# Kernel optimization log

Hardware: AMD Instinct MI355X
Metric: run time of the kernel (lower is better)

Reference implementation:

```python
import jax, jax.numpy as jnp
import numpy as np

B = 4096
IN_F = 4096
OUT_F = 4096
IN_Q = IN_F // 4
OUT_Q = OUT_F // 4


def setup_inputs() -> dict:
    key = jax.random.key(0)
    ks = jax.random.split(key, 9)
    scale = 1.0 / np.sqrt(IN_Q)
    inp = {"x": jax.random.normal(ks[0], (B, IN_F), dtype=jnp.float32)}
    for i, name in enumerate(["rr", "ri", "rj", "rk"]):
        inp[f"W_{name}"] = jax.random.uniform(ks[1 + i], (OUT_Q, IN_Q), dtype=jnp.float32, minval=-scale, maxval=scale)
        inp[f"b_{name}"] = jax.random.uniform(ks[5 + i], (OUT_Q,), dtype=jnp.float32, minval=-scale, maxval=scale)
    return inp


def reference(x, W_rr, W_ri, W_rj, W_rk, b_rr, b_ri, b_rj, b_rk):
    b = x.shape[0]
    # split into quaternion components: chunks c in {r,i,j,k}
    xs = x.reshape(b, 4, IN_Q)                       # [B, 4, IN_Q]
    W = jnp.stack([W_rr, W_ri, W_rj, W_rk])          # [4(lin), OUT_Q, IN_Q]
    bias = jnp.stack([b_rr, b_ri, b_rj, b_rk])       # [4(lin), OUT_Q]
    # all 16 linear applications in one batched GEMM: Y[b,c,q,:] = lin_q(x_c)
    Y = jnp.einsum('bci,qoi->bcqo', xs, W) + bias    # [B, 4, 4, OUT_Q]
    out_r = Y[:, 0, 0] - Y[:, 1, 1] - Y[:, 2, 2] - Y[:, 3, 3]
    out_i = Y[:, 0, 1] + Y[:, 1, 0] + Y[:, 2, 3] - Y[:, 3, 2]
    out_j = Y[:, 0, 2] - Y[:, 1, 3] + Y[:, 2, 0] + Y[:, 3, 1]
    out_k = Y[:, 0, 3] + Y[:, 1, 2] - Y[:, 2, 1] + Y[:, 3, 0]
    out = jnp.stack([out_r, out_i, out_j, out_k], axis=1)  # [B, 4, OUT_Q]
    return out.reshape(b, -1)                        # [B, OUT_F]
```

## Files before the change

kernel.cpp:

```cpp
#include <hip/hip_runtime.h>
#include <cstdint>
#include <cstddef>

#define MDIM 4096
#define NDIM 4096
#define KDIM 4096

typedef _Float16 half8  __attribute__((ext_vector_type(8)));
typedef float    floatx4 __attribute__((ext_vector_type(4)));

__device__ __constant__ int   d_qtab[16] = {0,1,2,3,  1,0,3,2,  2,3,0,1,  3,2,1,0};
__device__ __constant__ float d_stab[16] = {1.f,-1.f,-1.f,-1.f,
                                            1.f, 1.f, 1.f,-1.f,
                                            1.f,-1.f, 1.f, 1.f,
                                            1.f, 1.f,-1.f, 1.f};


__global__ void cast_x_kernel(const float* __restrict__ x, _Float16* __restrict__ xh) {
    int idx = blockIdx.x * 256 + threadIdx.x;
    const float4* src = (const float4*)x + (size_t)idx * 2;
    float4 a = src[0], b = src[1];
    half8 h = {(_Float16)a.x, (_Float16)a.y, (_Float16)a.z, (_Float16)a.w,
               (_Float16)b.x, (_Float16)b.y, (_Float16)b.z, (_Float16)b.w};
    ((half8*)xh)[idx] = h;
}

__global__ void cast_w_kernel(const float* __restrict__ W0, const float* __restrict__ W1,
                              const float* __restrict__ W2, const float* __restrict__ W3,
                              _Float16* __restrict__ Wh) {
    int idx = blockIdx.x * 256 + threadIdx.x;
    int e = idx << 3;
    int m = e >> 20;
    const float* Ws[4] = {W0, W1, W2, W3};
    const float* src = Ws[m] + (e & ((1 << 20) - 1));
    float4 a = *(const float4*)src;
    float4 b = *(const float4*)(src + 4);
    half8 h = {(_Float16)a.x, (_Float16)a.y, (_Float16)a.z, (_Float16)a.w,
               (_Float16)b.x, (_Float16)b.y, (_Float16)b.z, (_Float16)b.w};
    *(half8*)(Wh + e) = h;
}


__device__ __forceinline__ void gload_lds16(const _Float16* g, _Float16* l) {
    __builtin_amdgcn_global_load_lds(
        (const __attribute__((address_space(1))) unsigned int*)g,
        (__attribute__((address_space(3))) unsigned int*)l,
        16, 0, 0);
}

__global__ __launch_bounds__(256, 4) void gemm_kernel(
        const _Float16* __restrict__ A,
        const _Float16* __restrict__ Wh,
        const float* __restrict__ b0, const float* __restrict__ b1,
        const float* __restrict__ b2, const float* __restrict__ b3,
        float* __restrict__ C) {
    __shared__ _Float16 As[128 * 32];
    __shared__ _Float16 Bs[128 * 32];

    const int tid  = threadIdx.x;
    const int lane = tid & 63;
    const int wave = tid >> 6;
    const int wm = (wave & 1) * 64;
    const int wn = (wave >> 1) * 64;

    const int g = blockIdx.x;
    const int group_id = g >> 8;
    const int bm = group_id * 8 + (g & 7);
    const int bn = (g & 255) >> 3;
    const int m0 = bm * 128;
    const int n0 = bn * 128;
    const int comp = n0 >> 10;

    const int srow = tid >> 2;
    const int skc  = (((tid & 3) ^ ((srow >> 1) & 3))) * 8;
    const _Float16* Ag0 = A + (size_t)(m0 + srow) * KDIM + skc;
    const int brow = (n0 & 1023) + srow;

    _Float16* Asl0 = As + tid * 8;
    _Float16* Asl1 = As + 2048 + tid * 8;
    _Float16* Bsl0 = Bs + tid * 8;
    _Float16* Bsl1 = Bs + 2048 + tid * 8;

    floatx4 acc[4][4];
#pragma unroll
    for (int i = 0; i < 4; i++)
#pragma unroll
        for (int j = 0; j < 4; j++)
            acc[i][j] = (floatx4){0.f, 0.f, 0.f, 0.f};

    const int fr = lane & 15;
    const int q  = lane >> 4;
    const int slot8 = (q ^ ((fr >> 1) & 3)) * 8;

    for (int c = 0; c < 4; c++) {
        const int t = comp * 4 + c;
        const _Float16* Bg0 = Wh + ((size_t)d_qtab[t] << 20) + (size_t)brow * 1024 + skc;
        const _Float16* Ag  = Ag0 + c * 1024;
        const _Float16 s = (_Float16)d_stab[t];
        half8 sv = {s, s, s, s, s, s, s, s};

        for (int kk = 0; kk < 1024; kk += 32) {
            gload_lds16(Ag + kk, Asl0);
            gload_lds16(Ag + (size_t)64 * KDIM + kk, Asl1);
            gload_lds16(Bg0 + kk, Bsl0);
            gload_lds16(Bg0 + (size_t)64 * 1024 + kk, Bsl1);
            __syncthreads();

            half8 af[4], bf[4];
#pragma unroll
            for (int i = 0; i < 4; i++) {
                af[i] = *(const half8*)(As + (wm + i * 16 + fr) * 32 + slot8) * sv;
                bf[i] = *(const half8*)(Bs + (wn + i * 16 + fr) * 32 + slot8);
            }
#pragma unroll
            for (int i = 0; i < 4; i++)
#pragma unroll
                for (int j = 0; j < 4; j++)
                    acc[i][j] = __builtin_amdgcn_mfma_f32_16x16x32_f16(af[i], bf[j], acc[i][j], 0, 0, 0);

            __syncthreads();
        }
    }

    const int col   = lane & 15;
    const int rquad = (lane >> 4) * 4;
    const float* bs[4] = {b0, b1, b2, b3};
#pragma unroll
    for (int j = 0; j < 4; j++) {
        const int gn = n0 + wn + j * 16 + col;
        const int o  = gn & 1023;
        float bv = 0.f;
#pragma unroll
        for (int c = 0; c < 4; c++)
            bv += d_stab[comp * 4 + c] * bs[d_qtab[comp * 4 + c]][o];
#pragma unroll
        for (int i = 0; i < 4; i++) {
            const int gmb = m0 + wm + i * 16 + rquad;
#pragma unroll
            for (int r = 0; r < 4; r++)
                C[(size_t)(gmb + r) * NDIM + gn] = acc[i][j][r] + bv;
        }
    }
}

__global__ void fallback_kernel(const float* __restrict__ x,
                                const float* __restrict__ W0, const float* __restrict__ W1,
                                const float* __restrict__ W2, const float* __restrict__ W3,
                                const float* __restrict__ b0, const float* __restrict__ b1,
                                const float* __restrict__ b2, const float* __restrict__ b3,
                                float* __restrict__ out) {
    int idx = blockIdx.x * 256 + threadIdx.x;
    int m = idx >> 12, n = idx & 4095;
    int comp = n >> 10, o = n & 1023;
    const float* Ws[4] = {W0, W1, W2, W3};
    const float* bs[4] = {b0, b1, b2, b3};
    float acc = 0.f;
    for (int c = 0; c < 4; c++) {
        int t = comp * 4 + c;
        const float* wr = Ws[d_qtab[t]] + (size_t)o * 1024;
        const float* xr = x + (size_t)m * 4096 + c * 1024;
        float s = d_stab[t];
        float dot = 0.f;
        for (int i = 0; i < 1024; i += 4) {
            float4 wv = *(const float4*)(wr + i);
            float4 xv = *(const float4*)(xr + i);
            dot += wv.x * xv.x + wv.y * xv.y + wv.z * xv.z + wv.w * xv.w;
        }
        acc += s * dot + s * bs[d_qtab[t]][o];
    }
    out[idx] = acc;
}

extern "C" void kernel_launch(void* const* d_in, const int* in_sizes, int n_in,
                              void* d_out, int out_size, void* d_ws, size_t ws_size,
                              hipStream_t stream) {
    const float* x = (const float*)d_in[0];
    const float* W[4];
    const float* b[4];
    int wi = 0, bi = 0;
    for (int i = 1; i < n_in && i < 9; i++) {
        if (in_sizes[i] > 4096) { if (wi < 4) W[wi++] = (const float*)d_in[i]; }
        else                    { if (bi < 4) b[bi++] = (const float*)d_in[i]; }
    }
    float* out = (float*)d_out;

    const size_t xh_elems = (size_t)MDIM * KDIM;
    const size_t wh_elems = (size_t)4 * 1024 * 1024;
    const size_t needed = (xh_elems + wh_elems) * 2;

    if (ws_size < needed) {
        fallback_kernel<<<(MDIM * NDIM) / 256, 256, 0, stream>>>(
            x, W[0], W[1], W[2], W[3], b[0], b[1], b[2], b[3], out);
        return;
    }

    _Float16* xh = (_Float16*)d_ws;
    _Float16* Wh = xh + xh_elems;

    cast_x_kernel<<<(MDIM * KDIM) / (256 * 8), 256, 0, stream>>>(x, xh);
    cast_w_kernel<<<(4 * 1024 * 1024) / (256 * 8), 256, 0, stream>>>(W[0], W[1], W[2], W[3], Wh);
    gemm_kernel<<<(MDIM / 128) * (NDIM / 128), 256, 0, stream>>>(
        xh, Wh, b[0], b[1], b[2], b[3], out);
}
```

Measured before the change: 298.9 us.

## Switch to 32x32x16 MFMA, pre-negate weights, and merge cast kernels

The GEMM inner loop moves from 16x16x32 MFMA tiles to 32x32x16 tiles, using 2x2 accumulators of 16 floats per wave with new LDS fragment addressing and a new epilogue mapping. The per-fragment sign multiply is dropped by storing a negated copy of the fp16 weights and picking the positive or negative copy per quaternion term. The two cast kernels are merged into one launch that also writes the negated weights. This cuts per-iteration VALU work, LDS reads and one launch, in exchange for doubling the fp16 weight workspace and the extra writes in the prepass.

```diff
diff --git a/kernel.cpp b/kernel.cpp
--- a/kernel.cpp
+++ b/kernel.cpp
@@ -6,38 +6,43 @@
 #define NDIM 4096
 #define KDIM 4096
 
-typedef _Float16 half8  __attribute__((ext_vector_type(8)));
-typedef float    floatx4 __attribute__((ext_vector_type(4)));
+typedef _Float16 half8   __attribute__((ext_vector_type(8)));
+typedef float    floatx16 __attribute__((ext_vector_type(16)));
 
 __device__ __constant__ int   d_qtab[16] = {0,1,2,3,  1,0,3,2,  2,3,0,1,  3,2,1,0};
+__device__ __constant__ int   d_negtab[16] = {0,1,1,1,  0,0,0,1,  0,1,0,0,  0,0,1,0};
 __device__ __constant__ float d_stab[16] = {1.f,-1.f,-1.f,-1.f,
                                             1.f, 1.f, 1.f,-1.f,
                                             1.f,-1.f, 1.f, 1.f,
                                             1.f, 1.f,-1.f, 1.f};
 
-
-__global__ void cast_x_kernel(const float* __restrict__ x, _Float16* __restrict__ xh) {
-    int idx = blockIdx.x * 256 + threadIdx.x;
-    const float4* src = (const float4*)x + (size_t)idx * 2;
-    float4 a = src[0], b = src[1];
-    half8 h = {(_Float16)a.x, (_Float16)a.y, (_Float16)a.z, (_Float16)a.w,
-               (_Float16)b.x, (_Float16)b.y, (_Float16)b.z, (_Float16)b.w};
-    ((half8*)xh)[idx] = h;
-}
-
-__global__ void cast_w_kernel(const float* __restrict__ W0, const float* __restrict__ W1,
-                              const float* __restrict__ W2, const float* __restrict__ W3,
-                              _Float16* __restrict__ Wh) {
-    int idx = blockIdx.x * 256 + threadIdx.x;
-    int e = idx << 3;
-    int m = e >> 20;
-    const float* Ws[4] = {W0, W1, W2, W3};
-    const float* src = Ws[m] + (e & ((1 << 20) - 1));
-    float4 a = *(const float4*)src;
-    float4 b = *(const float4*)(src + 4);
-    half8 h = {(_Float16)a.x, (_Float16)a.y, (_Float16)a.z, (_Float16)a.w,
-               (_Float16)b.x, (_Float16)b.y, (_Float16)b.z, (_Float16)b.w};
-    *(half8*)(Wh + e) = h;
+__global__ void prepass_kernel(const float* __restrict__ x,
+                               const float* __restrict__ W0, const float* __restrict__ W1,
+                               const float* __restrict__ W2, const float* __restrict__ W3,
+                               _Float16* __restrict__ xh, _Float16* __restrict__ Wh) {
+    int b = blockIdx.x;
+    if (b < 8192) {
+        int idx = b * 256 + threadIdx.x;
+        const float4* src = (const float4*)x + (size_t)idx * 2;
+        float4 a = src[0], v = src[1];
+        half8 h = {(_Float16)a.x, (_Float16)a.y, (_Float16)a.z, (_Float16)a.w,
+                   (_Float16)v.x, (_Float16)v.y, (_Float16)v.z, (_Float16)v.w};
+        ((half8*)xh)[idx] = h;
+    } else {
+        int idx = (b - 8192) * 256 + threadIdx.x;
+        int e = idx << 3;
+        int m = e >> 20;
+        int off = e & ((1 << 20) - 1);
+        const float* Ws[4] = {W0, W1, W2, W3};
+        const float* src = Ws[m] + off;
+        float4 a = *(const float4*)src;
+        float4 v = *(const float4*)(src + 4);
+        half8 hp = {(_Float16)a.x, (_Float16)a.y, (_Float16)a.z, (_Float16)a.w,
+                    (_Float16)v.x, (_Float16)v.y, (_Float16)v.z, (_Float16)v.w};
+        half8 hn = -hp;
+        *(half8*)(Wh + ((size_t)m << 20) + off)       = hp;
+        *(half8*)(Wh + ((size_t)(4 + m) << 20) + off) = hn;
+    }
 }
 
 
@@ -72,32 +77,34 @@
     const int comp = n0 >> 10;
 
     const int srow = tid >> 2;
-    const int skc  = (((tid & 3) ^ ((srow >> 1) & 3))) * 8;
+    const int q_ld = tid & 3;
+    const int swz  = (srow >> 1) & 3;
+    const int skc  = (q_ld ^ swz) * 8;
     const _Float16* Ag0 = A + (size_t)(m0 + srow) * KDIM + skc;
     const int brow = (n0 & 1023) + srow;
-
     _Float16* Asl0 = As + tid * 8;
     _Float16* Asl1 = As + 2048 + tid * 8;
     _Float16* Bsl0 = Bs + tid * 8;
     _Float16* Bsl1 = Bs + 2048 + tid * 8;
 
-    floatx4 acc[4][4];
-#pragma unroll
-    for (int i = 0; i < 4; i++)
-#pragma unroll
-        for (int j = 0; j < 4; j++)
-            acc[i][j] = (floatx4){0.f, 0.f, 0.f, 0.f};
-
-    const int fr = lane & 15;
-    const int q  = lane >> 4;
-    const int slot8 = (q ^ ((fr >> 1) & 3)) * 8;
+    floatx16 acc[2][2];
+#pragma unroll
+    for (int i = 0; i < 2; i++)
+#pragma unroll
+        for (int j = 0; j < 2; j++)
+            acc[i][j] = (floatx16)0.f;
+
+    const int fr  = lane & 31;
+    const int kh  = lane >> 5;
+    const int rsw = (fr >> 1) & 3;
+    const int slot_s0 = (((0) + kh) ^ rsw) * 8;
+    const int slot_s1 = (((2) + kh) ^ rsw) * 8;
 
     for (int c = 0; c < 4; c++) {
         const int t = comp * 4 + c;
-        const _Float16* Bg0 = Wh + ((size_t)d_qtab[t] << 20) + (size_t)brow * 1024 + skc;
+        const _Float16* Bg0 = Wh + ((size_t)(d_qtab[t] + (d_negtab[t] << 2)) << 20)
+                                 + (size_t)brow * 1024 + skc;
         const _Float16* Ag  = Ag0 + c * 1024;
-        const _Float16 s = (_Float16)d_stab[t];
-        half8 sv = {s, s, s, s, s, s, s, s};
 
         for (int kk = 0; kk < 1024; kk += 32) {
             gload_lds16(Ag + kk, Asl0);
@@ -106,39 +113,47 @@
             gload_lds16(Bg0 + (size_t)64 * 1024 + kk, Bsl1);
             __syncthreads();
 
-            half8 af[4], bf[4];
-#pragma unroll
-            for (int i = 0; i < 4; i++) {
-                af[i] = *(const half8*)(As + (wm + i * 16 + fr) * 32 + slot8) * sv;
-                bf[i] = *(const half8*)(Bs + (wn + i * 16 + fr) * 32 + slot8);
+            half8 af[2][2], bf[2][2];
+#pragma unroll
+            for (int i = 0; i < 2; i++) {
+                const _Float16* ar = As + (wm + i * 32 + fr) * 32;
+                const _Float16* br = Bs + (wn + i * 32 + fr) * 32;
+                af[i][0] = *(const half8*)(ar + slot_s0);
+                af[i][1] = *(const half8*)(ar + slot_s1);
+                bf[i][0] = *(const half8*)(br + slot_s0);
+                bf[i][1] = *(const half8*)(br + slot_s1);
             }
 #pragma unroll
-            for (int i = 0; i < 4; i++)
-#pragma unroll
-                for (int j = 0; j < 4; j++)
-                    acc[i][j] = __builtin_amdgcn_mfma_f32_16x16x32_f16(af[i], bf[j], acc[i][j], 0, 0, 0);
+            for (int s = 0; s < 2; s++)
+#pragma unroll
+                for (int i = 0; i < 2; i++)
+#pragma unroll
+                    for (int j = 0; j < 2; j++)
+                        acc[i][j] = __builtin_amdgcn_mfma_f32_32x32x16_f16(
+                            af[i][s], bf[j][s], acc[i][j], 0, 0, 0);
 
             __syncthreads();
         }
     }
 
-    const int col   = lane & 15;
-    const int rquad = (lane >> 4) * 4;
+    const int col = lane & 31;
     const float* bs[4] = {b0, b1, b2, b3};
 #pragma unroll
-    for (int j = 0; j < 4; j++) {
-        const int gn = n0 + wn + j * 16 + col;
+    for (int j = 0; j < 2; j++) {
+        const int gn = n0 + wn + j * 32 + col;
         const int o  = gn & 1023;
         float bv = 0.f;
 #pragma unroll
         for (int c = 0; c < 4; c++)
             bv += d_stab[comp * 4 + c] * bs[d_qtab[comp * 4 + c]][o];
 #pragma unroll
-        for (int i = 0; i < 4; i++) {
-            const int gmb = m0 + wm + i * 16 + rquad;
-#pragma unroll
-            for (int r = 0; r < 4; r++)
-                C[(size_t)(gmb + r) * NDIM + gn] = acc[i][j][r] + bv;
+        for (int i = 0; i < 2; i++) {
+            const int gmb = m0 + wm + i * 32 + 4 * kh;
+#pragma unroll
+            for (int reg = 0; reg < 16; reg++) {
+                const int row = (reg & 3) + 8 * (reg >> 2);
+                C[(size_t)(gmb + row) * NDIM + gn] = acc[i][j][reg] + bv;
+            }
         }
     }
 }
@@ -185,7 +200,7 @@
     float* out = (float*)d_out;
 
     const size_t xh_elems = (size_t)MDIM * KDIM;
-    const size_t wh_elems = (size_t)4 * 1024 * 1024;
+    const size_t wh_elems = (size_t)8 * 1024 * 1024;
     const size_t needed = (xh_elems + wh_elems) * 2;
 
     if (ws_size < needed) {
@@ -197,8 +212,7 @@
     _Float16* xh = (_Float16*)d_ws;
     _Float16* Wh = xh + xh_elems;
 
-    cast_x_kernel<<<(MDIM * KDIM) / (256 * 8), 256, 0, stream>>>(x, xh);
-    cast_w_kernel<<<(4 * 1024 * 1024) / (256 * 8), 256, 0, stream>>>(W[0], W[1], W[2], W[3], Wh);
+    prepass_kernel<<<8192 + 2048, 256, 0, stream>>>(x, W[0], W[1], W[2], W[3], xh, Wh);
     gemm_kernel<<<(MDIM / 128) * (NDIM / 128), 256, 0, stream>>>(
         xh, Wh, b[0], b[1], b[2], b[3], out);
 }
```

Result: slower. 314.7 us (+5.3%).

## Double K-tile depth to 64 with new LDS swizzle and merge cast kernels

Applied to the files above, without the earlier changes.

The GEMM now stages a 128x64 K-slice of each operand per barrier pair instead of 128x32. Each thread issues four direct-to-LDS loads per operand, and the XOR swizzle is redone for the 8-chunk rows. Each wave runs two MFMA sub-steps per barrier, halving the number of synchronisations and load rounds per K, at the cost of double the LDS per block (32 KB), which may cap occupancy. The two fp32-to-fp16 cast kernels are also merged into one launch to save a kernel launch and tail.

```diff
diff --git a/kernel.cpp b/kernel.cpp
--- a/kernel.cpp
+++ b/kernel.cpp
@@ -6,7 +6,7 @@
 #define NDIM 4096
 #define KDIM 4096
 
-typedef _Float16 half8  __attribute__((ext_vector_type(8)));
+typedef _Float16 half8   __attribute__((ext_vector_type(8)));
 typedef float    floatx4 __attribute__((ext_vector_type(4)));
 
 __device__ __constant__ int   d_qtab[16] = {0,1,2,3,  1,0,3,2,  2,3,0,1,  3,2,1,0};
@@ -15,29 +15,31 @@
                                             1.f,-1.f, 1.f, 1.f,
                                             1.f, 1.f,-1.f, 1.f};
 
-
-__global__ void cast_x_kernel(const float* __restrict__ x, _Float16* __restrict__ xh) {
-    int idx = blockIdx.x * 256 + threadIdx.x;
-    const float4* src = (const float4*)x + (size_t)idx * 2;
-    float4 a = src[0], b = src[1];
-    half8 h = {(_Float16)a.x, (_Float16)a.y, (_Float16)a.z, (_Float16)a.w,
-               (_Float16)b.x, (_Float16)b.y, (_Float16)b.z, (_Float16)b.w};
-    ((half8*)xh)[idx] = h;
-}
-
-__global__ void cast_w_kernel(const float* __restrict__ W0, const float* __restrict__ W1,
-                              const float* __restrict__ W2, const float* __restrict__ W3,
-                              _Float16* __restrict__ Wh) {
-    int idx = blockIdx.x * 256 + threadIdx.x;
-    int e = idx << 3;
-    int m = e >> 20;
-    const float* Ws[4] = {W0, W1, W2, W3};
-    const float* src = Ws[m] + (e & ((1 << 20) - 1));
-    float4 a = *(const float4*)src;
-    float4 b = *(const float4*)(src + 4);
-    half8 h = {(_Float16)a.x, (_Float16)a.y, (_Float16)a.z, (_Float16)a.w,
-               (_Float16)b.x, (_Float16)b.y, (_Float16)b.z, (_Float16)b.w};
-    *(half8*)(Wh + e) = h;
+__global__ void prepass_kernel(const float* __restrict__ x,
+                               const float* __restrict__ W0, const float* __restrict__ W1,
+                               const float* __restrict__ W2, const float* __restrict__ W3,
+                               _Float16* __restrict__ xh, _Float16* __restrict__ Wh) {
+    int b = blockIdx.x;
+    if (b < 8192) {
+        int idx = b * 256 + threadIdx.x;
+        const float4* src = (const float4*)x + (size_t)idx * 2;
+        float4 a = src[0], v = src[1];
+        half8 h = {(_Float16)a.x, (_Float16)a.y, (_Float16)a.z, (_Float16)a.w,
+                   (_Float16)v.x, (_Float16)v.y, (_Float16)v.z, (_Float16)v.w};
+        ((half8*)xh)[idx] = h;
+    } else {
+        int idx = (b - 8192) * 256 + threadIdx.x;
+        int e = idx << 3;
+        int m = e >> 20;
+        int off = e & ((1 << 20) - 1);
+        const float* Ws[4] = {W0, W1, W2, W3};
+        const float* src = Ws[m] + off;
+        float4 a = *(const float4*)src;
+        float4 v = *(const float4*)(src + 4);
+        half8 h = {(_Float16)a.x, (_Float16)a.y, (_Float16)a.z, (_Float16)a.w,
+                   (_Float16)v.x, (_Float16)v.y, (_Float16)v.z, (_Float16)v.w};
+        *(half8*)(Wh + ((size_t)m << 20) + off) = h;
+    }
 }
 
 
@@ -54,8 +56,8 @@
         const float* __restrict__ b0, const float* __restrict__ b1,
         const float* __restrict__ b2, const float* __restrict__ b3,
         float* __restrict__ C) {
-    __shared__ _Float16 As[128 * 32];
-    __shared__ _Float16 Bs[128 * 32];
+    __shared__ _Float16 As[128 * 64];
+    __shared__ _Float16 Bs[128 * 64];
 
     const int tid  = threadIdx.x;
     const int lane = tid & 63;
@@ -71,15 +73,10 @@
     const int n0 = bn * 128;
     const int comp = n0 >> 10;
 
-    const int srow = tid >> 2;
-    const int skc  = (((tid & 3) ^ ((srow >> 1) & 3))) * 8;
-    const _Float16* Ag0 = A + (size_t)(m0 + srow) * KDIM + skc;
-    const int brow = (n0 & 1023) + srow;
-
-    _Float16* Asl0 = As + tid * 8;
-    _Float16* Asl1 = As + 2048 + tid * 8;
-    _Float16* Bsl0 = Bs + tid * 8;
-    _Float16* Bsl1 = Bs + 2048 + tid * 8;
+    const int lrow = tid >> 3;
+    const int gch  = (tid & 7) ^ (lrow & 7);
+    const _Float16* Ag0 = A + (size_t)(m0 + lrow) * KDIM + gch * 8;
+    const int brow0 = (n0 & 1023) + lrow;
 
     floatx4 acc[4][4];
 #pragma unroll
@@ -89,34 +86,43 @@
             acc[i][j] = (floatx4){0.f, 0.f, 0.f, 0.f};
 
     const int fr = lane & 15;
-    const int q  = lane >> 4;
-    const int slot8 = (q ^ ((fr >> 1) & 3)) * 8;
+    const int qf = lane >> 4;
+    const int fsw = fr & 7;
+    const int slot_s0 = (((0) + qf) ^ fsw) * 8;
+    const int slot_s1 = (((4) + qf) ^ fsw) * 8;
 
     for (int c = 0; c < 4; c++) {
         const int t = comp * 4 + c;
-        const _Float16* Bg0 = Wh + ((size_t)d_qtab[t] << 20) + (size_t)brow * 1024 + skc;
+        const _Float16* Bg0 = Wh + ((size_t)d_qtab[t] << 20)
+                                 + (size_t)brow0 * 1024 + gch * 8;
         const _Float16* Ag  = Ag0 + c * 1024;
         const _Float16 s = (_Float16)d_stab[t];
         half8 sv = {s, s, s, s, s, s, s, s};
 
-        for (int kk = 0; kk < 1024; kk += 32) {
-            gload_lds16(Ag + kk, Asl0);
-            gload_lds16(Ag + (size_t)64 * KDIM + kk, Asl1);
-            gload_lds16(Bg0 + kk, Bsl0);
-            gload_lds16(Bg0 + (size_t)64 * 1024 + kk, Bsl1);
+        for (int kk = 0; kk < 1024; kk += 64) {
+#pragma unroll
+            for (int r = 0; r < 4; r++) {
+                gload_lds16(Ag + kk + (size_t)r * 32 * KDIM, As + r * 2048 + tid * 8);
+                gload_lds16(Bg0 + kk + (size_t)r * 32 * 1024, Bs + r * 2048 + tid * 8);
+            }
             __syncthreads();
 
-            half8 af[4], bf[4];
-#pragma unroll
-            for (int i = 0; i < 4; i++) {
-                af[i] = *(const half8*)(As + (wm + i * 16 + fr) * 32 + slot8) * sv;
-                bf[i] = *(const half8*)(Bs + (wn + i * 16 + fr) * 32 + slot8);
+#pragma unroll
+            for (int s2 = 0; s2 < 2; s2++) {
+                const int slot = s2 ? slot_s1 : slot_s0;
+                half8 af[4], bf[4];
+#pragma unroll
+                for (int i = 0; i < 4; i++) {
+                    af[i] = *(const half8*)(As + (wm + i * 16 + fr) * 64 + slot) * sv;
+                    bf[i] = *(const half8*)(Bs + (wn + i * 16 + fr) * 64 + slot);
+                }
+#pragma unroll
+                for (int i = 0; i < 4; i++)
+#pragma unroll
+                    for (int j = 0; j < 4; j++)
+                        acc[i][j] = __builtin_amdgcn_mfma_f32_16x16x32_f16(
+                            af[i], bf[j], acc[i][j], 0, 0, 0);
             }
-#pragma unroll
-            for (int i = 0; i < 4; i++)
-#pragma unroll
-                for (int j = 0; j < 4; j++)
-                    acc[i][j] = __builtin_amdgcn_mfma_f32_16x16x32_f16(af[i], bf[j], acc[i][j], 0, 0, 0);
 
             __syncthreads();
         }
@@ -197,8 +203,7 @@
     _Float16* xh = (_Float16*)d_ws;
     _Float16* Wh = xh + xh_elems;
 
-    cast_x_kernel<<<(MDIM * KDIM) / (256 * 8), 256, 0, stream>>>(x, xh);
-    cast_w_kernel<<<(4 * 1024 * 1024) / (256 * 8), 256, 0, stream>>>(W[0], W[1], W[2], W[3], Wh);
+    prepass_kernel<<<8192 + 2048, 256, 0, stream>>>(x, W[0], W[1], W[2], W[3], xh, Wh);
     gemm_kernel<<<(MDIM / 128) * (NDIM / 128), 256, 0, stream>>>(
         xh, Wh, b[0], b[1], b[2], b[3], out);
 }
```

After: 279.3 us. -6.6%, faster.
